# Performance work log

Measured on AMD Instinct MI355X. Metric: run time of the kernel, lower is better.

Reference implementation:

```python
import jax, jax.numpy as jnp
import numpy as np

EPS = 1e-5  # torch BatchNorm2d default eps (eval mode with running stats)


def bn(x, g, b, m, v):
    # x: [B,C,H,W]; per-channel affine batchnorm in inference form
    return (x - m[:, None, None]) * (g[:, None, None] / jnp.sqrt(v[:, None, None] + EPS)) + b[:, None, None]


def self_attn(x, Wq, bq, Wk, bk, Wv, bv, rel_h, rel_w):
    # x: [B,C,H,W]; Wq/Wk/Wv: [C,C] (1x1 convs); rel_h: [C,H]; rel_w: [C,W]
    B, C, H, W = x.shape
    N = H * W
    q = jnp.einsum('oc,bchw->bohw', Wq, x).reshape(B, C, N) + bq[None, :, None]
    k = jnp.einsum('oc,bchw->bohw', Wk, x).reshape(B, C, N) + bk[None, :, None]
    v = jnp.einsum('oc,bchw->bohw', Wv, x).reshape(B, C, N) + bv[None, :, None]
    energy = jnp.einsum('bcn,bcm->bnm', q, k)                      # content: Q^T K
    pos = (rel_h[:, :, None] + rel_w[:, None, :]).reshape(C, N)    # [C, H*W]
    energy = energy + jnp.einsum('bcn,cm->bnm', q, pos)            # rel-pos bias term
    attn = jax.nn.softmax(energy, axis=-1)                         # [B,N,N]
    out = jnp.einsum('bcm,bnm->bcn', v, attn)                      # V @ attn^T
    return out.reshape(B, C, H, W)


def conv3x3(x, w):
    return jax.lax.conv_general_dilated(x, w, (1, 1), 'SAME',
                                        dimension_numbers=('NCHW', 'OIHW', 'NCHW'))


def setup_inputs() -> dict:
    key = jax.random.key(0)
    B, C, H, W, NH = 32, 512, 16, 16, 5
    ks = jax.random.split(key, 32)
    f = lambda i, shape, s=1.0: jax.random.normal(ks[i], shape, jnp.float32) * s
    inp = {
        'x0': f(0, (B, C, H, W)), 'x1': f(1, (B, C, H, W)), 'x2': f(2, (B, C, H, W)),
        'x3': f(3, (B, C, H, W)), 'x': f(4, (B, C, H, W)),
        'qW': f(5, (NH, C, C), 0.02), 'qB': f(6, (NH, C), 0.02),
        'kW': f(7, (NH, C, C), 0.02), 'kB': f(8, (NH, C), 0.02),
        'vW': f(9, (NH, C, C), 0.02), 'vB': f(10, (NH, C), 0.02),
        'relH': f(11, (NH, C, H)), 'relW': f(12, (NH, C, W)),
        'msw_W': f(13, (NH - 1, NH * C), 0.02),
        'msw_g': jnp.ones((NH - 1,)), 'msw_b': jnp.zeros((NH - 1,)),
        'msw_m': jnp.zeros((NH - 1,)), 'msw_v': jnp.ones((NH - 1,)),
        'fus_W': f(14, (C, C, 3, 3), 0.02),
        'fus_g': jnp.ones((C,)), 'fus_b': jnp.zeros((C,)),
        'fus_m': jnp.zeros((C,)), 'fus_v': jnp.ones((C,)),
        'top_g': jnp.ones((C,)), 'top_b': jnp.zeros((C,)),
        'top_m': jnp.zeros((C,)), 'top_v': jnp.ones((C,)),
        'h': 16, 'w': 16,
    }
    return inp


def reference(x0, x1, x2, x3, x, qW, qB, kW, kB, vW, vB, relH, relW,
              msw_W, msw_g, msw_b, msw_m, msw_v,
              fus_W, fus_g, fus_b, fus_m, fus_v,
              top_g, top_b, top_m, top_v, h, w):
    B, C, H, W = x.shape
    xs = jnp.stack([x0, x1, x2, x3, x])                            # [5,B,C,H,W]
    outs = jax.vmap(self_attn)(xs, qW, qB, kW, kB, vW, vB, relH, relW)  # [5,B,C,H,W]
    cat = outs.transpose(1, 0, 2, 3, 4).reshape(B, 5 * C, H, W)
    weights = jax.nn.sigmoid(bn(jnp.einsum('oc,bchw->bohw', msw_W, cat),
                                msw_g, msw_b, msw_m, msw_v))        # [B,4,H,W]
    x_ms = (weights[:, 0:1] * outs[0] + weights[:, 1:2] * outs[1]
            + weights[:, 2:3] * outs[2] + weights[:, 3:4] * outs[3] + outs[4])
    x_ms = jax.nn.relu(bn(conv3x3(x_ms, fus_W), fus_g, fus_b, fus_m, fus_v))
    out = jax.nn.relu(bn(x_ms + x, top_g, top_b, top_m, top_v))
    return out
```

## Files before the change

### kernel.cpp

```cpp
#include <hip/hip_runtime.h>
#include <cstdint>

using bf16x8  = __attribute__((ext_vector_type(8))) __bf16;
using f32x4   = __attribute__((ext_vector_type(4))) float;
using ushort8 = __attribute__((ext_vector_type(8))) unsigned short;

#define EPSN 1e-5f

__device__ __forceinline__ void gld16(const void* g, void* l) {
  __builtin_amdgcn_global_load_lds((const __attribute__((address_space(1))) void*)g,
                                   (__attribute__((address_space(3))) void*)l, 16, 0, 0);
}

__device__ __forceinline__ ushort f2bf(float f) {
  __bf16 h = (__bf16)f;
  return __builtin_bit_cast(unsigned short, h);
}
__device__ __forceinline__ float bf2f(ushort u) {
  union { uint32_t u; float f; } v; v.u = ((uint32_t)u) << 16; return v.f;
}

__device__ __forceinline__ void gemm_core(const ushort* __restrict__ Ag,
                                          const ushort* __restrict__ Bg,
                                          int ldk, int ksteps,
                                          ushort* As, ushort* Bs,
                                          f32x4 (&acc)[4][4]) {
  const int t = threadIdx.x, lane = t & 63, w = t >> 6;
  const int wr = w >> 1, wc = w & 1;
  for (int kt = 0; kt < ksteps; ++kt) {
    const int kbase = kt * 64;
#pragma unroll
    for (int p = 0; p < 4; ++p) {
      int q = p * 256 + t;
      int row = q >> 3, slot = q & 7;
      int srcs = slot ^ (row & 7);
      gld16(Ag + (size_t)row * ldk + kbase + srcs * 8, As + (p * 256 + w * 64) * 8);
      gld16(Bg + (size_t)row * ldk + kbase + srcs * 8, Bs + (p * 256 + w * 64) * 8);
    }
    __syncthreads();
#pragma unroll
    for (int kk = 0; kk < 2; ++kk) {
      bf16x8 af[4], bfv[4];
#pragma unroll
      for (int i = 0; i < 4; ++i) {
        int ra = wr * 64 + i * 16 + (lane & 15);
        int sa = (kk * 4 + (lane >> 4)) ^ (ra & 7);
        af[i] = *(const bf16x8*)(As + ra * 64 + sa * 8);
        int rb = wc * 64 + i * 16 + (lane & 15);
        int sb = (kk * 4 + (lane >> 4)) ^ (rb & 7);
        bfv[i] = *(const bf16x8*)(Bs + rb * 64 + sb * 8);
      }
#pragma unroll
      for (int i = 0; i < 4; ++i)
#pragma unroll
        for (int j = 0; j < 4; ++j)
          acc[i][j] = __builtin_amdgcn_mfma_f32_16x16x32_bf16(af[i], bfv[j], acc[i][j], 0, 0, 0);
    }
    __syncthreads();
  }
}

__global__ __launch_bounds__(256) void k_pre(const float* __restrict__ x0,
                                             const float* __restrict__ x1,
                                             const float* __restrict__ x2,
                                             const float* __restrict__ x3,
                                             const float* __restrict__ x4,
                                             const float* __restrict__ qW,
                                             const float* __restrict__ kW,
                                             const float* __restrict__ vW,
                                             const float* __restrict__ relH,
                                             const float* __restrict__ relW,
                                             ushort* __restrict__ xT,
                                             ushort* __restrict__ Wb,
                                             ushort* __restrict__ posb) {
  __shared__ float tile[64][65];
  int bid = blockIdx.x;
  const int t = threadIdx.x;
  if (bid < 5120) {
    const int nt4 = bid & 3;  bid >>= 2;
    const int ct  = bid & 7;  bid >>= 3;
    const int b   = bid & 31; bid >>= 5;
    const int ix  = bid;
    const float* xs = ix == 0 ? x0 : ix == 1 ? x1 : ix == 2 ? x2 : ix == 3 ? x3 : x4;
    const float* src = xs + ((size_t)b * 512 + ct * 64) * 256 + nt4 * 64;
    const int col = t & 63, rq = t >> 6;
#pragma unroll
    for (int rr = 0; rr < 16; ++rr) {
      int row = rr * 4 + rq;
      tile[row][col] = src[(size_t)row * 256 + col];
    }
    __syncthreads();
    ushort* dst = xT + ((size_t)(ix * 32 + b) * 256 + nt4 * 64) * 512 + ct * 64;
#pragma unroll
    for (int rr = 0; rr < 16; ++rr) {
      int nrow = rr * 4 + rq;
      dst[(size_t)nrow * 512 + col] = f2bf(tile[col][nrow]);
    }
  } else if (bid < 8960) {
    int idx = (bid - 5120) * 256 + t;
    int gi = idx * 4;
    int sel = gi / 1310720;
    int off = gi - sel * 1310720;
    const float* src = sel == 0 ? qW : (sel == 1 ? kW : vW);
    float4 vv = *(const float4*)(src + off);
    int h = off / 262144, rest = off - h * 262144;
    ushort4 o;
    o.x = f2bf(vv.x); o.y = f2bf(vv.y); o.z = f2bf(vv.z); o.w = f2bf(vv.w);
    *(ushort4*)(Wb + (size_t)(h * 3 + sel) * 262144 + rest) = o;
  } else {
    int idx8 = (bid - 8960) * 256 + t;
    int e0 = idx8 * 8;
    int c0 = e0 & 511, m = (e0 >> 9) & 255, h = e0 >> 17;
    ushort8 o;
#pragma unroll
    for (int e = 0; e < 8; ++e) {
      int c = c0 + e;
      o[e] = f2bf(relH[((size_t)h * 512 + c) * 16 + (m >> 4)] +
                  relW[((size_t)h * 512 + c) * 16 + (m & 15)]);
    }
    *(ushort8*)(posb + e0) = o;
  }
}

__global__ __launch_bounds__(256) void k_qkv(const ushort* __restrict__ Wb,
                                             const ushort* __restrict__ xT,
                                             const ushort* __restrict__ posb,
                                             const float* __restrict__ qB,
                                             const float* __restrict__ kB,
                                             const float* __restrict__ vB,
                                             ushort* __restrict__ qT,
                                             ushort* __restrict__ kpT,
                                             ushort* __restrict__ vv) {
  __shared__ ushort lds[128 * 148];
  ushort* As = lds;
  ushort* Bs = lds + 8192;
  int bid = blockIdx.x;
  bid = (bid & 7) * 480 + (bid >> 3);
  const int h = bid / 768;
  const int r = bid % 768;
  const int t = threadIdx.x, lane = t & 63, w = t >> 6;
  const int wr = w >> 1, wc = w & 1, g = lane >> 4, l = lane & 15;

  f32x4 acc[4][4];
#pragma unroll
  for (int i = 0; i < 4; ++i)
#pragma unroll
    for (int j = 0; j < 4; ++j) acc[i][j] = f32x4{0.f, 0.f, 0.f, 0.f};

  if (r < 512) {
    const int pt = r >> 3, ot = r & 7;
    const bool isq = ot < 4;
    const ushort* Ag = xT + ((size_t)h * 8192 + pt * 128) * 512;
    const ushort* Bg = Wb + ((size_t)(h * 3 + (isq ? 0 : 1)) * 512 + (ot & 3) * 128) * 512;
    gemm_core(Ag, Bg, 512, 8, As, Bs, acc);

    const float* bias = (isq ? qB : kB) + h * 512 + (ot & 3) * 128;
    float bj[4];
#pragma unroll
    for (int j = 0; j < 4; ++j) bj[j] = bias[wc * 64 + j * 16 + l];
    ushort(*Cs)[148] = (ushort(*)[148])lds;
#pragma unroll
    for (int i = 0; i < 4; ++i)
#pragma unroll
      for (int j = 0; j < 4; ++j)
#pragma unroll
        for (int rr = 0; rr < 4; ++rr)
          Cs[wr * 64 + i * 16 + g * 4 + rr][wc * 64 + j * 16 + l] = f2bf(acc[i][j][rr] + bj[j]);
    __syncthreads();
    ushort* dst = isq ? qT : kpT;
#pragma unroll
    for (int it = 0; it < 8; ++it) {
      int lin = it * 256 + t;
      int row = lin >> 4, cc = (lin & 15) * 8;
      int pglob = pt * 128 + row;
      ushort8 cv = *(const ushort8*)&Cs[row][cc];
      if (!isq) {
        ushort8 pv = *(const ushort8*)(posb + ((size_t)h * 256 + (pglob & 255)) * 512 +
                                       (ot & 3) * 128 + cc);
#pragma unroll
        for (int e = 0; e < 8; ++e) cv[e] = f2bf(bf2f(cv[e]) + bf2f(pv[e]));
      }
      *(ushort8*)(dst + ((size_t)h * 8192 + pglob) * 512 + (ot & 3) * 128 + cc) = cv;
    }
  } else {
    const int r2 = r - 512;
    const int mt = r2 >> 6, ntp = r2 & 63;
    const ushort* Ag = Wb + ((size_t)(h * 3 + 2) * 512 + mt * 128) * 512;
    const ushort* Bg = xT + ((size_t)h * 8192 + ntp * 128) * 512;
    gemm_core(Ag, Bg, 512, 8, As, Bs, acc);

    const float* biasv = vB + h * 512 + mt * 128;
    ushort(*Cs)[148] = (ushort(*)[148])lds;
#pragma unroll
    for (int i = 0; i < 4; ++i)
#pragma unroll
      for (int rr = 0; rr < 4; ++rr) {
        int oloc = wr * 64 + i * 16 + g * 4 + rr;
        float bv = biasv[oloc];
#pragma unroll
        for (int j = 0; j < 4; ++j)
          Cs[oloc][wc * 64 + j * 16 + l] = f2bf(acc[i][j][rr] + bv);
      }
    __syncthreads();
    const int b = ntp >> 1, nb = (ntp & 1) * 128;
#pragma unroll
    for (int it = 0; it < 8; ++it) {
      int lin = it * 256 + t;
      int row = lin >> 4, cc = (lin & 15) * 8;
      ushort8 cv = *(const ushort8*)&Cs[row][cc];
      *(ushort8*)(vv + (((size_t)(h * 32 + b)) * 512 + mt * 128 + row) * 256 + nb + cc) = cv;
    }
  }
}

__global__ __launch_bounds__(256) void k_attn(const ushort* __restrict__ qT,
                                              const ushort* __restrict__ kpT,
                                              const float* __restrict__ fusW,
                                              ushort* __restrict__ attn,
                                              ushort* __restrict__ Wconv) {
  __shared__ ushort sm[20480];
  __shared__ float red[4][64];
  __shared__ float comb[64];
  int bid = blockIdx.x;
  const int t = threadIdx.x;
  if (bid >= 640) {
    int p = (bid - 640) * 256 + t;
    const float* src = fusW + (size_t)p * 9;
    float vv[9];
#pragma unroll
    for (int s = 0; s < 9; ++s) vv[s] = src[s];
#pragma unroll
    for (int s = 0; s < 9; ++s) Wconv[(size_t)s * 262144 + p] = f2bf(vv[s]);
    return;
  }
  bid = (bid & 7) * 80 + (bid >> 3);
  const int rt = bid & 3;
  const int hb = bid >> 2;
  ushort* As = sm;
  ushort* Bs = sm + 4096;
  const ushort* Ag = qT + ((size_t)hb * 256 + rt * 64) * 512;
  const ushort* Bg = kpT + (size_t)hb * 256 * 512;
  const int lane = t & 63, w = t >> 6, g = lane >> 4, l = lane & 15;

  f32x4 acc[4][4];
#pragma unroll
  for (int i = 0; i < 4; ++i)
#pragma unroll
    for (int j = 0; j < 4; ++j) acc[i][j] = f32x4{0.f, 0.f, 0.f, 0.f};

  for (int kt = 0; kt < 8; ++kt) {
    const int kbase = kt * 64;
#pragma unroll
    for (int p = 0; p < 2; ++p) {
      int q = p * 256 + t;
      int row = q >> 3, slot = q & 7, srcs = slot ^ (row & 7);
      gld16(Ag + (size_t)row * 512 + kbase + srcs * 8, As + (p * 256 + w * 64) * 8);
    }
#pragma unroll
    for (int p = 0; p < 8; ++p) {
      int q = p * 256 + t;
      int row = q >> 3, slot = q & 7, srcs = slot ^ (row & 7);
      gld16(Bg + (size_t)row * 512 + kbase + srcs * 8, Bs + (p * 256 + w * 64) * 8);
    }
    __syncthreads();
#pragma unroll
    for (int kk = 0; kk < 2; ++kk) {
      bf16x8 af[4], bfv[4];
#pragma unroll
      for (int i = 0; i < 4; ++i) {
        int ra = i * 16 + l;
        int sa = (kk * 4 + g) ^ (ra & 7);
        af[i] = *(const bf16x8*)(As + ra * 64 + sa * 8);
        int rb = w * 64 + i * 16 + l;
        int sb = (kk * 4 + g) ^ (rb & 7);
        bfv[i] = *(const bf16x8*)(Bs + rb * 64 + sb * 8);
      }
#pragma unroll
      for (int i = 0; i < 4; ++i)
#pragma unroll
        for (int j = 0; j < 4; ++j)
          acc[i][j] = __builtin_amdgcn_mfma_f32_16x16x32_bf16(af[i], bfv[j], acc[i][j], 0, 0, 0);
    }
    __syncthreads();
  }

#pragma unroll
  for (int i = 0; i < 4; ++i)
#pragma unroll
    for (int rr = 0; rr < 4; ++rr) {
      float v = fmaxf(fmaxf(acc[i][0][rr], acc[i][1][rr]), fmaxf(acc[i][2][rr], acc[i][3][rr]));
#pragma unroll
      for (int m = 1; m < 16; m <<= 1) v = fmaxf(v, __shfl_xor(v, m));
      if (l == 0) red[w][i * 16 + g * 4 + rr] = v;
    }
  __syncthreads();
  if (t < 64) comb[t] = fmaxf(fmaxf(red[0][t], red[1][t]), fmaxf(red[2][t], red[3][t]));
  __syncthreads();
#pragma unroll
  for (int i = 0; i < 4; ++i)
#pragma unroll
    for (int rr = 0; rr < 4; ++rr) {
      float mx = comb[i * 16 + g * 4 + rr];
      float s = 0.f;
#pragma unroll
      for (int j = 0; j < 4; ++j) {
        float e = expf(acc[i][j][rr] - mx);
        acc[i][j][rr] = e;
        s += e;
      }
#pragma unroll
      for (int m = 1; m < 16; m <<= 1) s += __shfl_xor(s, m);
      if (l == 0) red[w][i * 16 + g * 4 + rr] = s;
    }
  __syncthreads();
  if (t < 64) comb[t] = red[0][t] + red[1][t] + red[2][t] + red[3][t];
  __syncthreads();
  ushort(*P)[260] = (ushort(*)[260])sm;
#pragma unroll
  for (int i = 0; i < 4; ++i)
#pragma unroll
    for (int rr = 0; rr < 4; ++rr) {
      int row = i * 16 + g * 4 + rr;
      float inv = 1.f / comb[row];
#pragma unroll
      for (int j = 0; j < 4; ++j)
        P[row][w * 64 + j * 16 + l] = f2bf(acc[i][j][rr] * inv);
    }
  __syncthreads();
  ushort* Arow = attn + (size_t)hb * 65536 + (size_t)rt * 16384;
#pragma unroll
  for (int it = 0; it < 8; ++it) {
    int lin = it * 256 + t;
    int row = lin >> 5, c8 = (lin & 31) * 8;
    ushort8 cv = *(const ushort8*)&P[row][c8];
    *(ushort8*)(Arow + (size_t)row * 256 + c8) = cv;
  }
}

__global__ __launch_bounds__(256) void k_pv(const ushort* __restrict__ attn,
                                            const ushort* __restrict__ vv,
                                            ushort* __restrict__ OT) {
  __shared__ ushort lds[128 * 148];
  ushort* As = lds;
  ushort* Bs = lds + 8192;
  int bid = blockIdx.x;
  bid = (bid & 7) * 160 + (bid >> 3);
  const int nt = bid & 3; bid >>= 2;
  const int mt = bid & 1; bid >>= 1;
  const size_t hb = (size_t)bid;
  const ushort* Ag = attn + (hb * 256 + mt * 128) * 256;
  const ushort* Bg = vv + (hb * 512 + nt * 128) * 256;
  f32x4 acc[4][4];
#pragma unroll
  for (int i = 0; i < 4; ++i)
#pragma unroll
    for (int j = 0; j < 4; ++j) acc[i][j] = f32x4{0.f, 0.f, 0.f, 0.f};
  gemm_core(Ag, Bg, 256, 4, As, Bs, acc);
  const int t = threadIdx.x, lane = t & 63, w = t >> 6;
  const int wr = w >> 1, wc = w & 1, g = lane >> 4, l = lane & 15;
  ushort(*Cs)[148] = (ushort(*)[148])lds;
#pragma unroll
  for (int i = 0; i < 4; ++i)
#pragma unroll
    for (int j = 0; j < 4; ++j)
#pragma unroll
      for (int rr = 0; rr < 4; ++rr)
        Cs[wr * 64 + i * 16 + g * 4 + rr][wc * 64 + j * 16 + l] = f2bf(acc[i][j][rr]);
  __syncthreads();
#pragma unroll
  for (int it = 0; it < 8; ++it) {
    int lin = it * 256 + t;
    int row = lin >> 4, cc = (lin & 15) * 8;
    ushort8 cv = *(const ushort8*)&Cs[row][cc];
    *(ushort8*)(OT + (hb * 256 + mt * 128 + row) * 512 + nt * 128 + cc) = cv;
  }
}

__global__ __launch_bounds__(256) void k_weights(const ushort* __restrict__ OT,
                                                 const float* __restrict__ mswW,
                                                 const float* __restrict__ mg,
                                                 const float* __restrict__ mb,
                                                 const float* __restrict__ mm,
                                                 const float* __restrict__ mv,
                                                 ushort* __restrict__ xmsT) {
  __shared__ float msw[10240];
  const int t = threadIdx.x, lane = t & 63, w = t >> 6;
#pragma unroll
  for (int it = 0; it < 10; ++it) {
    int idx = it * 1024 + t * 4;
    *(float4*)(msw + idx) = *(const float4*)(mswW + idx);
  }
  __syncthreads();
  const size_t pix = (size_t)blockIdx.x * 4 + w;
  float o[5][2][4];
#pragma unroll
  for (int h = 0; h < 5; ++h)
#pragma unroll
    for (int hf = 0; hf < 2; ++hf) {
      ushort4 v = *(const ushort4*)(OT + ((size_t)h * 8192 + pix) * 512 + hf * 256 + lane * 4);
      o[h][hf][0] = bf2f(v.x); o[h][hf][1] = bf2f(v.y);
      o[h][hf][2] = bf2f(v.z); o[h][hf][3] = bf2f(v.w);
    }
  float a[4] = {0.f, 0.f, 0.f, 0.f};
#pragma unroll
  for (int j = 0; j < 4; ++j)
#pragma unroll
    for (int h = 0; h < 5; ++h)
#pragma unroll
      for (int hf = 0; hf < 2; ++hf) {
        float4 m4 = *(const float4*)(msw + j * 2560 + h * 512 + hf * 256 + lane * 4);
        a[j] += m4.x * o[h][hf][0] + m4.y * o[h][hf][1] +
                m4.z * o[h][hf][2] + m4.w * o[h][hf][3];
      }
#pragma unroll
  for (int m = 1; m < 64; m <<= 1) {
    a[0] += __shfl_xor(a[0], m); a[1] += __shfl_xor(a[1], m);
    a[2] += __shfl_xor(a[2], m); a[3] += __shfl_xor(a[3], m);
  }
  float wj[4];
#pragma unroll
  for (int j = 0; j < 4; ++j) {
    float val = (a[j] - mm[j]) * (mg[j] * rsqrtf(mv[j] + EPSN)) + mb[j];
    wj[j] = 1.f / (1.f + expf(-val));
  }
#pragma unroll
  for (int hf = 0; hf < 2; ++hf) {
    ushort4 ov;
    float* op = (float*)&ov;
    float r0 = wj[0] * o[0][hf][0] + wj[1] * o[1][hf][0] + wj[2] * o[2][hf][0] + wj[3] * o[3][hf][0] + o[4][hf][0];
    float r1 = wj[0] * o[0][hf][1] + wj[1] * o[1][hf][1] + wj[2] * o[2][hf][1] + wj[3] * o[3][hf][1] + o[4][hf][1];
    float r2 = wj[0] * o[0][hf][2] + wj[1] * o[1][hf][2] + wj[2] * o[2][hf][2] + wj[3] * o[3][hf][2] + o[4][hf][2];
    float r3 = wj[0] * o[0][hf][3] + wj[1] * o[1][hf][3] + wj[2] * o[2][hf][3] + wj[3] * o[3][hf][3] + o[4][hf][3];
    ushort4 pk; pk.x = f2bf(r0); pk.y = f2bf(r1); pk.z = f2bf(r2); pk.w = f2bf(r3);
    *(ushort4*)(xmsT + pix * 512 + hf * 256 + lane * 4) = pk;
  }
  (void)0;
}

__global__ __launch_bounds__(256) void k_conv(const ushort* __restrict__ Wconv,
                                              const ushort* __restrict__ xmsT,
                                              float* __restrict__ y1a,
                                              float* __restrict__ y1b) {
  __shared__ ushort As3[3 * 128 * 64];
  __shared__ ushort xp[180 * 76];
  int bid = blockIdx.x;
  bid = (bid & 7) * 64 + (bid >> 3);
  const int ntl = bid & 1; bid >>= 1;
  const int mt = bid & 3;  bid >>= 2;
  const int halfk = bid & 1; bid >>= 1;
  const int bb = bid;
  const int y0 = ntl * 8;
  const int t = threadIdx.x, lane = t & 63, w = t >> 6, wr = w >> 1, wc = w & 1;
  f32x4 acc[4][4];
#pragma unroll
  for (int i = 0; i < 4; ++i)
#pragma unroll
    for (int j = 0; j < 4; ++j) acc[i][j] = f32x4{0.f, 0.f, 0.f, 0.f};

  for (int cb = halfk * 4; cb < halfk * 4 + 4; ++cb) {
    __syncthreads();
    for (int u = t; u < 1440; u += 256) {
      int slot = u & 7;
      int xpi = (u >> 3) % 18;
      int rl = u / 144;
      int yg = y0 - 1 + rl, xg = xpi - 1;
      uint4 val = make_uint4(0, 0, 0, 0);
      if (yg >= 0 && yg < 16 && (unsigned)xg < 16u)
        val = *(const uint4*)(xmsT + ((size_t)bb * 256 + yg * 16 + xg) * 512 + cb * 64 + slot * 8);
      *(uint4*)(xp + (rl * 18 + xpi) * 76 + slot * 8) = val;
    }
    for (int dy = 0; dy < 3; ++dy) {
#pragma unroll
      for (int dx = 0; dx < 3; ++dx)
#pragma unroll
        for (int p = 0; p < 4; ++p) {
          int q = p * 256 + t;
          int row = q >> 3, slot = q & 7, srcs = slot ^ (row & 7);
          gld16(Wconv + ((size_t)(dy * 3 + dx) * 512 + mt * 128 + row) * 512 + cb * 64 + srcs * 8,
                As3 + dx * 8192 + (p * 256 + w * 64) * 8);
        }
      __syncthreads();
#pragma unroll
      for (int dx = 0; dx < 3; ++dx)
#pragma unroll
        for (int kk = 0; kk < 2; ++kk) {
          bf16x8 af[4], bfv[4];
#pragma unroll
          for (int i = 0; i < 4; ++i) {
            int ra = wr * 64 + i * 16 + (lane & 15);
            int sa = (kk * 4 + (lane >> 4)) ^ (ra & 7);
            af[i] = *(const bf16x8*)(As3 + dx * 8192 + ra * 64 + sa * 8);
            int nl = wc * 64 + i * 16 + (lane & 15);
            int pp = ((nl >> 4) + dy) * 18 + (nl & 15) + dx;
            bfv[i] = *(const bf16x8*)(xp + pp * 76 + (kk * 4 + (lane >> 4)) * 8);
          }
#pragma unroll
          for (int i = 0; i < 4; ++i)
#pragma unroll
            for (int j = 0; j < 4; ++j)
              acc[i][j] = __builtin_amdgcn_mfma_f32_16x16x32_bf16(af[i], bfv[j], acc[i][j], 0, 0, 0);
        }
      __syncthreads();
    }
  }
  float* yp = halfk ? y1b : y1a;
  const int o0 = mt * 128 + wr * 64 + ((lane >> 4) << 2);
  const int n0 = ntl * 128 + wc * 64 + (lane & 15);
#pragma unroll
  for (int i = 0; i < 4; ++i)
#pragma unroll
    for (int j = 0; j < 4; ++j)
#pragma unroll
      for (int rr = 0; rr < 4; ++rr) {
        int o = o0 + i * 16 + rr, n = n0 + j * 16;
        yp[((size_t)bb * 512 + o) * 256 + n] = acc[i][j][rr];
      }
}

__global__ __launch_bounds__(256) void k_top(const float* __restrict__ y1a,
                                             const float* __restrict__ y1b,
                                             const float* __restrict__ x,
                                             const float* __restrict__ fg,
                                             const float* __restrict__ fb,
                                             const float* __restrict__ fm,
                                             const float* __restrict__ fv,
                                             const float* __restrict__ tg,
                                             const float* __restrict__ tb,
                                             const float* __restrict__ tm,
                                             const float* __restrict__ tv,
                                             float* __restrict__ out) {
  size_t i4 = ((size_t)blockIdx.x * 256 + threadIdx.x) * 4;
  int c = (int)((i4 >> 8) & 511);
  float4 a = *(const float4*)(y1a + i4);
  float4 bq = *(const float4*)(y1b + i4);
  float4 xx = *(const float4*)(x + i4);
  float sf = fg[c] * rsqrtf(fv[c] + EPSN), mf = fm[c], bf_ = fb[c];
  float st = tg[c] * rsqrtf(tv[c] + EPSN), mt_ = tm[c], bt_ = tb[c];
  float4 o;
  float v;
  v = fmaxf((a.x + bq.x - mf) * sf + bf_, 0.f); o.x = fmaxf((v + xx.x - mt_) * st + bt_, 0.f);
  v = fmaxf((a.y + bq.y - mf) * sf + bf_, 0.f); o.y = fmaxf((v + xx.y - mt_) * st + bt_, 0.f);
  v = fmaxf((a.z + bq.z - mf) * sf + bf_, 0.f); o.z = fmaxf((v + xx.z - mt_) * st + bt_, 0.f);
  v = fmaxf((a.w + bq.w - mf) * sf + bf_, 0.f); o.w = fmaxf((v + xx.w - mt_) * st + bt_, 0.f);
  *(float4*)(out + i4) = o;
}

extern "C" void kernel_launch(void* const* d_in, const int* in_sizes, int n_in,
                              void* d_out, int out_size, void* d_ws, size_t ws_size,
                              hipStream_t stream) {
  const float* x0   = (const float*)d_in[0];
  const float* x1   = (const float*)d_in[1];
  const float* x2   = (const float*)d_in[2];
  const float* x3   = (const float*)d_in[3];
  const float* x4   = (const float*)d_in[4];
  const float* qW   = (const float*)d_in[5];
  const float* qB   = (const float*)d_in[6];
  const float* kW   = (const float*)d_in[7];
  const float* kB   = (const float*)d_in[8];
  const float* vW   = (const float*)d_in[9];
  const float* vB   = (const float*)d_in[10];
  const float* relH = (const float*)d_in[11];
  const float* relW = (const float*)d_in[12];
  const float* mswW = (const float*)d_in[13];
  const float* msg  = (const float*)d_in[14];
  const float* msb  = (const float*)d_in[15];
  const float* msm  = (const float*)d_in[16];
  const float* msv  = (const float*)d_in[17];
  const float* fusW = (const float*)d_in[18];
  const float* fg   = (const float*)d_in[19];
  const float* fb   = (const float*)d_in[20];
  const float* fm   = (const float*)d_in[21];
  const float* fv   = (const float*)d_in[22];
  const float* tg   = (const float*)d_in[23];
  const float* tb   = (const float*)d_in[24];
  const float* tm   = (const float*)d_in[25];
  const float* tv   = (const float*)d_in[26];

  if (ws_size < 180355072ull) return;
  char* ws = (char*)d_ws;
  ushort* xT    = (ushort*)(ws + 0);
  ushort* attn  = (ushort*)(ws + 0);
  ushort* Wconv = (ushort*)(ws + 20971520);
  ushort* qT    = (ushort*)(ws + 41943040);
  ushort* xmsT  = (ushort*)(ws + 41943040);
  float*  y1a   = (float*)(ws + 50331648);
  float*  y1b   = (float*)(ws + 67108864);
  ushort* kpT   = (ushort*)(ws + 83886080);
  ushort* OT    = (ushort*)(ws + 83886080);
  ushort* vv    = (ushort*)(ws + 125829120);
  ushort* Wb    = (ushort*)(ws + 167772160);
  ushort* posb  = (ushort*)(ws + 175636480);

  k_pre    <<<9280, 256, 0, stream>>>(x0, x1, x2, x3, x4, qW, kW, vW, relH, relW,
                                      xT, Wb, posb);
  k_qkv    <<<3840, 256, 0, stream>>>(Wb, xT, posb, qB, kB, vB, qT, kpT, vv);
  k_attn   <<<1664, 256, 0, stream>>>(qT, kpT, fusW, attn, Wconv);
  k_pv     <<<1280, 256, 0, stream>>>(attn, vv, OT);
  k_weights<<<2048, 256, 0, stream>>>(OT, mswW, msg, msb, msm, msv, xmsT);
  k_conv   <<<512,  256, 0, stream>>>(Wconv, xmsT, y1a, y1b);
  k_top    <<<4096, 256, 0, stream>>>(y1a, y1b, x4, fg, fb, fm, fv, tg, tb, tm, tv, (float*)d_out);
}
```

Baseline: 272.2 us.

## Rewrite QKV projection GEMM with 256x256 tiles and 4-stage LDS pipeline

After: 267.6 us. Within noise of the previous version (-1.7%).

```diff
diff --git a/kernel.cpp b/kernel.cpp
--- a/kernel.cpp
+++ b/kernel.cpp
@@ -122,95 +122,178 @@
   }
 }
 
-__global__ __launch_bounds__(256) void k_qkv(const ushort* __restrict__ Wb,
-                                             const ushort* __restrict__ xT,
-                                             const ushort* __restrict__ posb,
-                                             const float* __restrict__ qB,
-                                             const float* __restrict__ kB,
-                                             const float* __restrict__ vB,
-                                             ushort* __restrict__ qT,
-                                             ushort* __restrict__ kpT,
-                                             ushort* __restrict__ vv) {
-  __shared__ ushort lds[128 * 148];
-  ushort* As = lds;
-  ushort* Bs = lds + 8192;
+__global__ __launch_bounds__(512, 2) void k_qkv2(const ushort* __restrict__ Wb,
+                                                 const ushort* __restrict__ xT,
+                                                 const ushort* __restrict__ posb,
+                                                 const float* __restrict__ qB,
+                                                 const float* __restrict__ kB,
+                                                 const float* __restrict__ vB,
+                                                 ushort* __restrict__ qT,
+                                                 ushort* __restrict__ kpT,
+                                                 ushort* __restrict__ vv) {
+  extern __shared__ ushort ls[];
+  const int t = threadIdx.x, lane = t & 63;
+  const int w = t >> 6, wm = w >> 2, wn = w & 3, g = lane >> 4, l = lane & 15;
   int bid = blockIdx.x;
-  bid = (bid & 7) * 480 + (bid >> 3);
-  const int h = bid / 768;
-  const int r = bid % 768;
-  const int t = threadIdx.x, lane = t & 63, w = t >> 6;
-  const int wr = w >> 1, wc = w & 1, g = lane >> 4, l = lane & 15;
-
-  f32x4 acc[4][4];
-#pragma unroll
-  for (int i = 0; i < 4; ++i)
+  bid = (bid & 7) * 120 + (bid >> 3);
+  const int h = bid / 192;
+  const int r = bid % 192;
+
+  const ushort* Ag;
+  const ushort* Bg;
+  const bool partA = r < 128;
+  int pt = 0, nt = 0, mt = 0, ntv = 0;
+  if (partA) {
+    pt = r >> 2; nt = r & 3;
+    Ag = xT + ((size_t)h * 8192 + pt * 256) * 512;
+    const int sel = nt < 2 ? 0 : 1;
+    Bg = Wb + ((size_t)(h * 3 + sel) * 512 + (nt & 1) * 256) * 512;
+  } else {
+    const int r2 = r - 128;
+    mt = r2 >> 5; ntv = r2 & 31;
+    Ag = Wb + ((size_t)(h * 3 + 2) * 512 + mt * 256) * 512;
+    Bg = xT + ((size_t)h * 8192 + ntv * 256) * 512;
+  }
+
+  f32x4 acc[8][4];
+#pragma unroll
+  for (int i = 0; i < 8; ++i)
 #pragma unroll
     for (int j = 0; j < 4; ++j) acc[i][j] = f32x4{0.f, 0.f, 0.f, 0.f};
 
-  if (r < 512) {
-    const int pt = r >> 3, ot = r & 7;
-    const bool isq = ot < 4;
-    const ushort* Ag = xT + ((size_t)h * 8192 + pt * 128) * 512;
-    const ushort* Bg = Wb + ((size_t)(h * 3 + (isq ? 0 : 1)) * 512 + (ot & 3) * 128) * 512;
-    gemm_core(Ag, Bg, 512, 8, As, Bs, acc);
-
-    const float* bias = (isq ? qB : kB) + h * 512 + (ot & 3) * 128;
+#define QKV_STAGE(tt, slot)                                                    \
+  {                                                                            \
+    const int kb_ = (tt) * 32;                                                 \
+    ushort* sa_ = ls + (slot) * 8192;                                          \
+    ushort* sb_ = ls + 32768 + (slot) * 8192;                                  \
+    _Pragma("unroll")                                                          \
+    for (int p_ = 0; p_ < 2; ++p_) {                                           \
+      int q_ = p_ * 512 + t;                                                   \
+      int row_ = q_ >> 2, s4_ = q_ & 3;                                        \
+      int src_ = s4_ ^ ((row_ ^ (row_ >> 2)) & 3);                             \
+      gld16(Ag + (size_t)row_ * 512 + kb_ + src_ * 8, sa_ + q_ * 8);           \
+      gld16(Bg + (size_t)row_ * 512 + kb_ + src_ * 8, sb_ + q_ * 8);           \
+    }                                                                          \
+  }
+
+#define QKV_COMPUTE(slot)                                                      \
+  {                                                                            \
+    ushort* sa_ = ls + (slot) * 8192;                                          \
+    ushort* sb_ = ls + 32768 + (slot) * 8192;                                  \
+    bf16x8 bfv[4], af[8];                                                      \
+    _Pragma("unroll")                                                          \
+    for (int j_ = 0; j_ < 4; ++j_) {                                           \
+      int rb_ = wn * 64 + j_ * 16 + l;                                         \
+      int sb2_ = g ^ ((rb_ ^ (rb_ >> 2)) & 3);                                 \
+      bfv[j_] = *(const bf16x8*)(sb_ + rb_ * 32 + sb2_ * 8);                   \
+    }                                                                          \
+    _Pragma("unroll")                                                          \
+    for (int i_ = 0; i_ < 8; ++i_) {                                           \
+      int ra_ = wm * 128 + i_ * 16 + l;                                        \
+      int sa2_ = g ^ ((ra_ ^ (ra_ >> 2)) & 3);                                 \
+      af[i_] = *(const bf16x8*)(sa_ + ra_ * 32 + sa2_ * 8);                    \
+    }                                                                          \
+    asm volatile("s_waitcnt lgkmcnt(0)" ::: "memory");                         \
+    __builtin_amdgcn_sched_barrier(0);                                         \
+    __builtin_amdgcn_s_setprio(1);                                             \
+    _Pragma("unroll")                                                          \
+    for (int i_ = 0; i_ < 8; ++i_)                                             \
+      _Pragma("unroll")                                                        \
+      for (int j_ = 0; j_ < 4; ++j_)                                           \
+        acc[i_][j_] = __builtin_amdgcn_mfma_f32_16x16x32_bf16(af[i_], bfv[j_], \
+                                                              acc[i_][j_], 0, 0, 0); \
+    __builtin_amdgcn_s_setprio(0);                                             \
+  }
+
+  QKV_STAGE(0, 0);
+  QKV_STAGE(1, 1);
+  for (int tt = 0; tt < 14; ++tt) {
+    QKV_STAGE(tt + 2, (tt + 2) & 3);
+    __builtin_amdgcn_sched_barrier(0);
+    asm volatile("s_waitcnt vmcnt(8)" ::: "memory");
+    __builtin_amdgcn_s_barrier();
+    __builtin_amdgcn_sched_barrier(0);
+    QKV_COMPUTE(tt & 3);
+  }
+  __builtin_amdgcn_sched_barrier(0);
+  asm volatile("s_waitcnt vmcnt(4)" ::: "memory");
+  __builtin_amdgcn_s_barrier();
+  __builtin_amdgcn_sched_barrier(0);
+  QKV_COMPUTE(2);
+  __builtin_amdgcn_sched_barrier(0);
+  asm volatile("s_waitcnt vmcnt(0)" ::: "memory");
+  __builtin_amdgcn_s_barrier();
+  __builtin_amdgcn_sched_barrier(0);
+  QKV_COMPUTE(3);
+  __builtin_amdgcn_sched_barrier(0);
+  __syncthreads();
+
+  ushort(*Cs)[272] = (ushort(*)[272])ls;
+  if (partA) {
+    const bool isq = nt < 2;
+    const float* bias = (isq ? qB : kB) + (size_t)h * 512 + (nt & 1) * 256;
+    ushort* dst = isq ? qT : kpT;
     float bj[4];
 #pragma unroll
-    for (int j = 0; j < 4; ++j) bj[j] = bias[wc * 64 + j * 16 + l];
-    ushort(*Cs)[148] = (ushort(*)[148])lds;
-#pragma unroll
-    for (int i = 0; i < 4; ++i)
-#pragma unroll
-      for (int j = 0; j < 4; ++j)
-#pragma unroll
-        for (int rr = 0; rr < 4; ++rr)
-          Cs[wr * 64 + i * 16 + g * 4 + rr][wc * 64 + j * 16 + l] = f2bf(acc[i][j][rr] + bj[j]);
-    __syncthreads();
-    ushort* dst = isq ? qT : kpT;
-#pragma unroll
-    for (int it = 0; it < 8; ++it) {
-      int lin = it * 256 + t;
-      int row = lin >> 4, cc = (lin & 15) * 8;
-      int pglob = pt * 128 + row;
-      ushort8 cv = *(const ushort8*)&Cs[row][cc];
-      if (!isq) {
-        ushort8 pv = *(const ushort8*)(posb + ((size_t)h * 256 + (pglob & 255)) * 512 +
-                                       (ot & 3) * 128 + cc);
-#pragma unroll
-        for (int e = 0; e < 8; ++e) cv[e] = f2bf(bf2f(cv[e]) + bf2f(pv[e]));
-      }
-      *(ushort8*)(dst + ((size_t)h * 8192 + pglob) * 512 + (ot & 3) * 128 + cc) = cv;
+    for (int j = 0; j < 4; ++j) bj[j] = bias[wn * 64 + j * 16 + l];
+#pragma unroll
+    for (int R = 0; R < 2; ++R) {
+      if (wm == R) {
+#pragma unroll
+        for (int i = 0; i < 8; ++i)
+#pragma unroll
+          for (int j = 0; j < 4; ++j)
+#pragma unroll
+            for (int rr = 0; rr < 4; ++rr)
+              Cs[i * 16 + g * 4 + rr][wn * 64 + j * 16 + l] = f2bf(acc[i][j][rr] + bj[j]);
+      }
+      __syncthreads();
+#pragma unroll
+      for (int it = 0; it < 8; ++it) {
+        int lin = it * 512 + t;
+        int row = lin >> 5, cc8 = (lin & 31) * 8;
+        ushort8 cv = *(const ushort8*)&Cs[row][cc8];
+        if (!isq) {
+          ushort8 pv = *(const ushort8*)(posb + ((size_t)h * 256 + R * 128 + row) * 512 +
+                                         (nt & 1) * 256 + cc8);
+#pragma unroll
+          for (int e = 0; e < 8; ++e) cv[e] = f2bf(bf2f(cv[e]) + bf2f(pv[e]));
+        }
+        *(ushort8*)(dst + ((size_t)h * 8192 + pt * 256 + R * 128 + row) * 512 +
+                    (nt & 1) * 256 + cc8) = cv;
+      }
+      if (R == 0) __syncthreads();
     }
   } else {
-    const int r2 = r - 512;
-    const int mt = r2 >> 6, ntp = r2 & 63;
-    const ushort* Ag = Wb + ((size_t)(h * 3 + 2) * 512 + mt * 128) * 512;
-    const ushort* Bg = xT + ((size_t)h * 8192 + ntp * 128) * 512;
-    gemm_core(Ag, Bg, 512, 8, As, Bs, acc);
-
-    const float* biasv = vB + h * 512 + mt * 128;
-    ushort(*Cs)[148] = (ushort(*)[148])lds;
-#pragma unroll
-    for (int i = 0; i < 4; ++i)
-#pragma unroll
-      for (int rr = 0; rr < 4; ++rr) {
-        int oloc = wr * 64 + i * 16 + g * 4 + rr;
-        float bv = biasv[oloc];
-#pragma unroll
-        for (int j = 0; j < 4; ++j)
-          Cs[oloc][wc * 64 + j * 16 + l] = f2bf(acc[i][j][rr] + bv);
-      }
-    __syncthreads();
-    const int b = ntp >> 1, nb = (ntp & 1) * 128;
-#pragma unroll
-    for (int it = 0; it < 8; ++it) {
-      int lin = it * 256 + t;
-      int row = lin >> 4, cc = (lin & 15) * 8;
-      ushort8 cv = *(const ushort8*)&Cs[row][cc];
-      *(ushort8*)(vv + (((size_t)(h * 32 + b)) * 512 + mt * 128 + row) * 256 + nb + cc) = cv;
-    }
-  }
+    const float* bias = vB + (size_t)h * 512 + mt * 256;
+#pragma unroll
+    for (int R = 0; R < 2; ++R) {
+      if (wm == R) {
+#pragma unroll
+        for (int i = 0; i < 8; ++i) {
+          float4 b4 = *(const float4*)(bias + R * 128 + i * 16 + g * 4);
+#pragma unroll
+          for (int j = 0; j < 4; ++j)
+#pragma unroll
+            for (int rr = 0; rr < 4; ++rr)
+              Cs[i * 16 + g * 4 + rr][wn * 64 + j * 16 + l] =
+                  f2bf(acc[i][j][rr] + ((const float*)&b4)[rr]);
+        }
+      }
+      __syncthreads();
+#pragma unroll
+      for (int it = 0; it < 8; ++it) {
+        int lin = it * 512 + t;
+        int row = lin >> 5, cc8 = (lin & 31) * 8;
+        ushort8 cv = *(const ushort8*)&Cs[row][cc8];
+        *(ushort8*)(vv + (((size_t)(h * 32 + ntv)) * 512 + mt * 256 + R * 128 + row) * 256 +
+                    cc8) = cv;
+      }
+      if (R == 0) __syncthreads();
+    }
+  }
+#undef QKV_STAGE
+#undef QKV_COMPUTE
 }
 
 __global__ __launch_bounds__(256) void k_attn(const ushort* __restrict__ qT,
@@ -425,8 +508,6 @@
   }
 #pragma unroll
   for (int hf = 0; hf < 2; ++hf) {
-    ushort4 ov;
-    float* op = (float*)&ov;
     float r0 = wj[0] * o[0][hf][0] + wj[1] * o[1][hf][0] + wj[2] * o[2][hf][0] + wj[3] * o[3][hf][0] + o[4][hf][0];
     float r1 = wj[0] * o[0][hf][1] + wj[1] * o[1][hf][1] + wj[2] * o[2][hf][1] + wj[3] * o[3][hf][1] + o[4][hf][1];
     float r2 = wj[0] * o[0][hf][2] + wj[1] * o[1][hf][2] + wj[2] * o[2][hf][2] + wj[3] * o[3][hf][2] + o[4][hf][2];
@@ -434,7 +515,6 @@
     ushort4 pk; pk.x = f2bf(r0); pk.y = f2bf(r1); pk.z = f2bf(r2); pk.w = f2bf(r3);
     *(ushort4*)(xmsT + pix * 512 + hf * 256 + lane * 4) = pk;
   }
-  (void)0;
 }
 
 __global__ __launch_bounds__(256) void k_conv(const ushort* __restrict__ Wconv,
@@ -591,9 +671,12 @@
   ushort* Wb    = (ushort*)(ws + 167772160);
   ushort* posb  = (ushort*)(ws + 175636480);
 
+  hipFuncSetAttribute((const void*)k_qkv2,
+                      hipFuncAttributeMaxDynamicSharedMemorySize, 131072);
+
   k_pre    <<<9280, 256, 0, stream>>>(x0, x1, x2, x3, x4, qW, kW, vW, relH, relW,
                                       xT, Wb, posb);
-  k_qkv    <<<3840, 256, 0, stream>>>(Wb, xT, posb, qB, kB, vB, qT, kpT, vv);
+  k_qkv2   <<<960, 512, 131072, stream>>>(Wb, xT, posb, qB, kB, vB, qT, kpT, vv);
   k_attn   <<<1664, 256, 0, stream>>>(qT, kpT, fusW, attn, Wconv);
   k_pv     <<<1280, 256, 0, stream>>>(attn, vv, OT);
   k_weights<<<2048, 256, 0, stream>>>(OT, mswW, msg, msb, msm, msv, xmsT);
```
